# Kernel optimization log

Measured on AMD Instinct MI355X. Metric: run time of the kernel, lower is better.

The kernel has to match this reference:

```python
import jax, jax.numpy as jnp
import numpy as np

FEAT_STRIDE = 16
NUM_ANCHORS = 9
PRE_NMS_TOPN = 6000
POST_NMS_TOPN = 300
NMS_THRESH = 0.7
ANCHOR_SCALES = np.array([8.0, 16.0, 32.0])
ANCHOR_RATIOS = np.array([0.5, 1.0, 2.0])
BBOX_CLIP = float(np.log(1000.0 / 16.0))  # standard delta clip to avoid exp overflow


def _mkanchors(ws, hs, xc, yc):
    return np.stack([xc - 0.5 * (ws - 1), yc - 0.5 * (hs - 1),
                     xc + 0.5 * (ws - 1), yc + 0.5 * (hs - 1)], axis=1)


def _base_anchors(base_size=16):
    w = h = float(base_size)
    xc = yc = 0.5 * (base_size - 1)
    size = w * h
    ws = np.round(np.sqrt(size / ANCHOR_RATIOS))
    hs = np.round(ws * ANCHOR_RATIOS)
    ratio_anchors = _mkanchors(ws, hs, xc, yc)
    out = []
    for a in ratio_anchors:
        aw = a[2] - a[0] + 1.0
        ah = a[3] - a[1] + 1.0
        axc = a[0] + 0.5 * (aw - 1.0)
        ayc = a[1] + 0.5 * (ah - 1.0)
        out.append(_mkanchors(aw * ANCHOR_SCALES, ah * ANCHOR_SCALES, axc, ayc))
    return np.concatenate(out, axis=0)  # [A, 4]


def _all_anchors(H, W):
    base = _base_anchors(FEAT_STRIDE)
    sx = np.arange(W) * FEAT_STRIDE
    sy = np.arange(H) * FEAT_STRIDE
    shift_x, shift_y = np.meshgrid(sx, sy)  # row-major over (h, w)
    shifts = np.stack([shift_x.ravel(), shift_y.ravel(),
                       shift_x.ravel(), shift_y.ravel()], axis=1)
    return (shifts[:, None, :] + base[None, :, :]).reshape(-1, 4).astype(np.float32)


def _conv2d(x, w, b, pad):
    y = jax.lax.conv_general_dilated(x, w, (1, 1), [(pad, pad), (pad, pad)],
                                     dimension_numbers=("NCHW", "OIHW", "NCHW"))
    return y + b[None, :, None, None]


def _decode_clip(anchors, deltas, im_h, im_w):
    aw = anchors[:, 2] - anchors[:, 0] + 1.0
    ah = anchors[:, 3] - anchors[:, 1] + 1.0
    acx = anchors[:, 0] + 0.5 * aw
    acy = anchors[:, 1] + 0.5 * ah
    dx, dy = deltas[:, 0], deltas[:, 1]
    dw = jnp.clip(deltas[:, 2], -BBOX_CLIP, BBOX_CLIP)
    dh = jnp.clip(deltas[:, 3], -BBOX_CLIP, BBOX_CLIP)
    pcx = dx * aw + acx
    pcy = dy * ah + acy
    pw = jnp.exp(dw) * aw
    ph = jnp.exp(dh) * ah
    x1 = jnp.clip(pcx - 0.5 * pw, 0.0, im_w - 1.0)
    y1 = jnp.clip(pcy - 0.5 * ph, 0.0, im_h - 1.0)
    x2 = jnp.clip(pcx + 0.5 * pw, 0.0, im_w - 1.0)
    y2 = jnp.clip(pcy + 0.5 * ph, 0.0, im_h - 1.0)
    return jnp.stack([x1, y1, x2, y2], axis=1)


def _nms_suppressed(boxes, thresh):
    # boxes sorted by score descending; greedy NMS, returns bool suppression mask
    n = boxes.shape[0]
    idx = jnp.arange(n)
    areas = (boxes[:, 2] - boxes[:, 0] + 1.0) * (boxes[:, 3] - boxes[:, 1] + 1.0)
    def body(i, supp):
        b = boxes[i]
        iw = jnp.maximum(0.0, jnp.minimum(b[2], boxes[:, 2]) - jnp.maximum(b[0], boxes[:, 0]) + 1.0)
        ih = jnp.maximum(0.0, jnp.minimum(b[3], boxes[:, 3]) - jnp.maximum(b[1], boxes[:, 1]) + 1.0)
        inter = iw * ih
        iou = inter / (areas[i] + areas - inter)
        kill = (~supp[i]) & (iou > thresh) & (idx > i)
        return supp | kill
    return jax.lax.fori_loop(0, n, body, jnp.zeros((n,), jnp.bool_))


def reference(feature, im_info, w_rpn_conv, b_rpn_conv, w_score, b_score, w_bbox, b_bbox):
    N, C, H, W = feature.shape
    A = NUM_ANCHORS
    rpn_feat = _conv2d(feature, w_rpn_conv, b_rpn_conv, 1)             # [N,512,H,W]
    cls_logits = _conv2d(rpn_feat, w_score, b_score, 0)                # [N,2A,H,W]
    # _reshape_layer(x,2) + softmax(dim=1) + _reshape_layer(x,2A): channels [0:A]=bg, [A:2A]=fg
    fg_prob = jax.nn.softmax(cls_logits.reshape(N, 2, A, H, W), axis=1)[:, 1]  # [N,A,H,W]
    scores = fg_prob.transpose(0, 2, 3, 1).reshape(-1)                 # (h,w,a) order, matches anchors
    deltas = _conv2d(rpn_feat, w_bbox, b_bbox, 0).transpose(0, 2, 3, 1).reshape(-1, 4)
    anchors = jnp.asarray(_all_anchors(H, W))                          # [H*W*A, 4]
    im_h = im_info[0].astype(jnp.float32)
    im_w = im_info[1].astype(jnp.float32)
    proposals = _decode_clip(anchors, deltas, im_h, im_w)
    top_scores, order = jax.lax.top_k(scores, PRE_NMS_TOPN)            # sorted desc
    boxes = proposals[order]
    supp = _nms_suppressed(jax.lax.stop_gradient(boxes), NMS_THRESH)
    masked = jnp.where(supp, -1.0, jax.lax.stop_gradient(top_scores))
    _, keep = jax.lax.top_k(masked, POST_NMS_TOPN)                     # first POST_NMS survivors
    rois_boxes = boxes[keep]                                           # [300, 4]
    roi_scores = top_scores[keep][:, None]                             # [300, 1]
    rois = jnp.concatenate([jnp.zeros((POST_NMS_TOPN, 1), rois_boxes.dtype), rois_boxes], axis=1)
    return rois, roi_scores, feature


def setup_inputs() -> dict:
    key = jax.random.key(0)
    ks = jax.random.split(key, 4)
    C, H, W, A = 512, 128, 128, NUM_ANCHORS
    feature = jax.random.normal(ks[0], (1, C, H, W), jnp.float32)
    w_rpn_conv = jax.random.normal(ks[1], (512, C, 3, 3), jnp.float32) * 0.01
    b_rpn_conv = jnp.zeros((512,), jnp.float32)
    w_score = jax.random.normal(ks[2], (2 * A, 512, 1, 1), jnp.float32) * 0.01
    b_score = jnp.zeros((2 * A,), jnp.float32)
    w_bbox = jax.random.normal(ks[3], (4 * A, 512, 1, 1), jnp.float32) * 0.001
    b_bbox = jnp.zeros((4 * A,), jnp.float32)
    im_info = jnp.array([H * FEAT_STRIDE, W * FEAT_STRIDE, 1], jnp.int32)
    return {"feature": feature, "im_info": im_info,
            "w_rpn_conv": w_rpn_conv, "b_rpn_conv": b_rpn_conv,
            "w_score": w_score, "b_score": b_score,
            "w_bbox": w_bbox, "b_bbox": b_bbox}
```

## Files before the change

kernel.cpp:

```cpp
#include <hip/hip_runtime.h>
#include <hip/hip_bf16.h>


#define HH 128
#define WW 128
#define HW 16384
#define CC 512
#define NANCH 9
#define NTOT 147456
#define PRE_TOPN 6000
#define POST_TOPN 300
#define NMS_WORDS 94
#define CAND_CAP 16384

typedef unsigned int u32;
typedef unsigned long long u64;

__constant__ float c_anch[9][4] = {
  { -84.f,  -40.f,  99.f,  55.f},
  {-176.f,  -88.f, 191.f, 103.f},
  {-360.f, -184.f, 375.f, 199.f},
  { -56.f,  -56.f,  71.f,  71.f},
  {-120.f, -120.f, 135.f, 135.f},
  {-248.f, -248.f, 263.f, 263.f},
  { -36.f,  -80.f,  51.f,  95.f},
  { -80.f, -168.f,  95.f, 183.f},
  {-168.f, -344.f, 183.f, 351.f}
};

__global__ __launch_bounds__(256, 4)
void conv3x3(const float* __restrict__ feat, const float* __restrict__ wconv,
             const float* __restrict__ bias, float* __restrict__ out)
{
  __shared__ float sA[8][3][136];
  __shared__ float sW[72][64];
  const int tid  = threadIdx.x;
  const int oc0  = (blockIdx.x & 7) << 6;
  const int r    = blockIdx.x >> 3;
  const int ocg  = tid >> 4;
  const int p    = tid & 15;

  if (tid < 48) {
    int ic = tid / 6, rm = tid % 6;
    sA[ic][rm >> 1][(rm & 1) ? 132 : 3] = 0.f;
  }

  double acc[4][8];
  #pragma unroll
  for (int o = 0; o < 4; ++o) {
    double bv = (double)bias[oc0 + ocg * 4 + o];
    #pragma unroll
    for (int j = 0; j < 8; ++j) acc[o][j] = bv;
  }

  for (int ic0 = 0; ic0 < CC; ic0 += 8) {
    __syncthreads();
    #pragma unroll
    for (int k = 0; k < 3; ++k) {
      int s   = tid + 256 * k;
      int icr = s >> 5;
      int ic  = icr / 3, rr = icr % 3;
      int c4  = (s & 31) << 2;
      int grow = r - 1 + rr;
      float4 v = make_float4(0.f, 0.f, 0.f, 0.f);
      if (grow >= 0 && grow < HH)
        v = *reinterpret_cast<const float4*>(&feat[(ic0 + ic) * HW + grow * WW + c4]);
      *reinterpret_cast<float4*>(&sA[ic][rr][4 + c4]) = v;
    }
    {
      int oc = tid & 63, part = tid >> 6;
      const float* wp = &wconv[(size_t)((oc0 + oc) * CC + ic0) * 9 + part * 18];
      #pragma unroll
      for (int k = 0; k < 18; ++k) sW[part * 18 + k][oc] = wp[k];
    }
    __syncthreads();

    for (int ic = 0; ic < 8; ++ic) {
      #pragma unroll
      for (int ky = 0; ky < 3; ++ky) {
        double w[3][4];
        #pragma unroll
        for (int kx = 0; kx < 3; ++kx)
          #pragma unroll
          for (int o = 0; o < 4; ++o)
            w[kx][o] = (double)sW[ic * 9 + ky * 3 + kx][ocg * 4 + o];
        const float* arow = &sA[ic][ky][4];
        #pragma unroll
        for (int j = 0; j < 8; ++j) {
          int c = p + 16 * j;
          double a0 = (double)arow[c - 1];
          double a1 = (double)arow[c];
          double a2 = (double)arow[c + 1];
          #pragma unroll
          for (int o = 0; o < 4; ++o) {
            acc[o][j] = fma(a0, w[0][o], acc[o][j]);
            acc[o][j] = fma(a1, w[1][o], acc[o][j]);
            acc[o][j] = fma(a2, w[2][o], acc[o][j]);
          }
        }
      }
    }
  }

  #pragma unroll
  for (int o = 0; o < 4; ++o) {
    float* op = &out[(size_t)(oc0 + ocg * 4 + o) * HW + r * WW];
    #pragma unroll
    for (int j = 0; j < 8; ++j)
      op[p + 16 * j] = (float)acc[o][j];
  }
}

__global__ __launch_bounds__(256, 2)
void conv1x1_decode(const float* __restrict__ rfeat, const float* __restrict__ wsc,
                    const float* __restrict__ bsc, const float* __restrict__ wbb,
                    const float* __restrict__ bbb, const int* __restrict__ im_info,
                    float* __restrict__ scores, double4* __restrict__ props,
                    u32* __restrict__ hist)
{
  __shared__ float  sA[32][64];
  __shared__ float  sW[32][56];
  __shared__ double sOut[64][56];
  const int tid  = threadIdx.x;
  const int px0  = blockIdx.x * 64;
  const int q    = tid >> 6;
  const int px_l = tid & 63;
  const int o0   = q * 14;

  double acc[14];
  #pragma unroll
  for (int o = 0; o < 14; ++o) {
    int oo = o0 + o;
    float b = 0.f;
    if (oo < 18) b = bsc[oo];
    else if (oo < 54) b = bbb[oo - 18];
    acc[o] = (double)b;
  }

  for (int ic0 = 0; ic0 < CC; ic0 += 32) {
    __syncthreads();
    #pragma unroll
    for (int k = 0; k < 2; ++k) {
      int s  = tid + 256 * k;
      int ic = s >> 4;
      int c4 = (s & 15) << 2;
      *reinterpret_cast<float4*>(&sA[ic][c4]) =
        *reinterpret_cast<const float4*>(&rfeat[(ic0 + ic) * HW + px0 + c4]);
    }
    for (int idx = tid; idx < 32 * 56; idx += 256) {
      int ic = idx / 56, o = idx % 56;
      float v = 0.f;
      if (o < 18) v = wsc[o * CC + ic0 + ic];
      else if (o < 54) v = wbb[(o - 18) * CC + ic0 + ic];
      sW[ic][o] = v;
    }
    __syncthreads();
    for (int ic = 0; ic < 32; ++ic) {
      double a = (double)sA[ic][px_l];
      #pragma unroll
      for (int o = 0; o < 14; ++o)
        acc[o] = fma(a, (double)sW[ic][o0 + o], acc[o]);
    }
  }
  #pragma unroll
  for (int o = 0; o < 14; ++o) sOut[px_l][o0 + o] = acc[o];
  __syncthreads();

  const double im_h = (double)im_info[0];
  const double im_w = (double)im_info[1];
  const double BCLIP = 4.1351665567423557;
  for (int t = tid; t < 64 * NANCH; t += 256) {
    int pl = t / 9, a = t % 9;
    int gp = px0 + pl;
    double l0 = sOut[pl][a], l1 = sOut[pl][9 + a];
    double sc = 1.0 / (1.0 + exp(l0 - l1));
    float scf = (float)sc;
    int gi = gp * 9 + a;
    scores[gi] = scf;
    atomicAdd(&hist[__float_as_uint(scf) >> 16], 1u);

    double dx = sOut[pl][18 + 4 * a + 0];
    double dy = sOut[pl][18 + 4 * a + 1];
    double dw = sOut[pl][18 + 4 * a + 2];
    double dh = sOut[pl][18 + 4 * a + 3];
    int wq = gp & 127, hq = gp >> 7;
    double ax1 = (double)c_anch[a][0] + 16.0 * wq;
    double ay1 = (double)c_anch[a][1] + 16.0 * hq;
    double ax2 = (double)c_anch[a][2] + 16.0 * wq;
    double ay2 = (double)c_anch[a][3] + 16.0 * hq;
    double aw = ax2 - ax1 + 1.0, ah = ay2 - ay1 + 1.0;
    double acx = ax1 + 0.5 * aw,  acy = ay1 + 0.5 * ah;
    dw = fmin(fmax(dw, -BCLIP), BCLIP);
    dh = fmin(fmax(dh, -BCLIP), BCLIP);
    double pcx = dx * aw + acx, pcy = dy * ah + acy;
    double pw = exp(dw) * aw,   ph = exp(dh) * ah;
    double x1 = fmin(fmax(pcx - 0.5 * pw, 0.0), im_w - 1.0);
    double y1 = fmin(fmax(pcy - 0.5 * ph, 0.0), im_h - 1.0);
    double x2 = fmin(fmax(pcx + 0.5 * pw, 0.0), im_w - 1.0);
    double y2 = fmin(fmax(pcy + 0.5 * ph, 0.0), im_h - 1.0);
    props[gi] = make_double4(x1, y1, x2, y2);
  }
}

__global__ __launch_bounds__(1024)
void scan_hist(const u32* __restrict__ hist, u32* __restrict__ scal)
{
  __shared__ u32 suf[1024];
  const int t = threadIdx.x;
  u32 s = 0;
  for (int k = 0; k < 64; ++k) s += hist[t * 64 + k];
  suf[t] = s;
  __syncthreads();
  for (int off = 1; off < 1024; off <<= 1) {
    u32 v = (t + off < 1024) ? suf[t + off] : 0u;
    __syncthreads();
    suf[t] += v;
    __syncthreads();
  }
  u32 here = suf[t];
  u32 next = (t < 1023) ? suf[t + 1] : 0u;
  if (here >= PRE_TOPN && (t == 1023 || next < PRE_TOPN)) {
    u32 cum = next;
    int T = t * 64;
    for (int b = 63; b >= 0; --b) {
      cum += hist[t * 64 + b];
      if (cum >= PRE_TOPN) { T = t * 64 + b; break; }
    }
    scal[1] = (u32)T;
  }
}

__global__ void compact_cand(const float* __restrict__ scores,
                             u32* __restrict__ scal, u64* __restrict__ cand)
{
  int t = blockIdx.x * 256 + threadIdx.x;
  if (t >= NTOT) return;
  u32 bits = __float_as_uint(scores[t]);
  if ((bits >> 16) >= scal[1]) {
    u32 pos = atomicAdd(&scal[0], 1u);
    if (pos < CAND_CAP)
      cand[pos] = ((u64)bits << 32) | (u64)(0xFFFFFFFFu - (u32)t);
  }
}

__global__ __launch_bounds__(1024)
void sort_topk(const u64* __restrict__ cand, const u32* __restrict__ scal,
               const double4* __restrict__ props, float* __restrict__ tscore,
               double4* __restrict__ boxes)
{
  __shared__ u64 sk[CAND_CAP];
  u32 n = scal[0]; if (n > CAND_CAP) n = CAND_CAP;
  const int SZ = (n <= 8192) ? 8192 : CAND_CAP;
  for (int t = threadIdx.x; t < SZ; t += 1024)
    sk[t] = (t < (int)n) ? cand[t] : 0ull;
  __syncthreads();
  for (int k = 2; k <= SZ; k <<= 1)
    for (int j = k >> 1; j > 0; j >>= 1) {
      for (int t = threadIdx.x; t < SZ; t += 1024) {
        int p = t ^ j;
        if (p > t) {
          u64 va = sk[t], vb = sk[p];
          bool sw = ((t & k) == 0) ? (va < vb) : (va > vb);
          if (sw) { sk[t] = vb; sk[p] = va; }
        }
      }
      __syncthreads();
    }
  for (int t = threadIdx.x; t < PRE_TOPN; t += 1024) {
    u64 key = sk[t];
    u32 idx = 0xFFFFFFFFu - (u32)key;
    tscore[t] = __uint_as_float((u32)(key >> 32));
    boxes[t]  = props[idx];
  }
}

__global__ __launch_bounds__(64)
void nms_mask(const double4* __restrict__ boxes, u64* __restrict__ mask)
{
  const int bi = blockIdx.y, bj = blockIdx.x;
  const int t = threadIdx.x;
  const int i = bi * 64 + t;
  if (bj < bi) { if (i < PRE_TOPN) mask[(u32)i * NMS_WORDS + bj] = 0ull; return; }
  __shared__ double4 cb[64];
  __shared__ double  ca[64];
  const int j0 = bj * 64;
  if (j0 + t < PRE_TOPN) {
    double4 b = boxes[j0 + t];
    cb[t] = b;
    ca[t] = (b.z - b.x + 1.0) * (b.w - b.y + 1.0);
  }
  __syncthreads();
  if (i >= PRE_TOPN) return;
  double4 bb = boxes[i];
  double ai = (bb.z - bb.x + 1.0) * (bb.w - bb.y + 1.0);
  const int jmax = min(64, PRE_TOPN - j0);
  u64 word = 0ull;
  for (int jj = 0; jj < jmax; ++jj) {
    int j = j0 + jj;
    if (j <= i) continue;
    double4 cj = cb[jj];
    double iw = fmin(bb.z, cj.z) - fmax(bb.x, cj.x) + 1.0;
    double ih = fmin(bb.w, cj.w) - fmax(bb.y, cj.y) + 1.0;
    iw = fmax(iw, 0.0); ih = fmax(ih, 0.0);
    double inter = iw * ih;
    double iou = inter / (ai + ca[jj] - inter);
    if (iou > 0.7) word |= (1ull << jj);
  }
  mask[(u32)i * NMS_WORDS + bj] = word;
}

__global__ __launch_bounds__(256)
void nms_finalize(const u64* __restrict__ mask, const double4* __restrict__ boxes,
                  const float* __restrict__ tscore, float* __restrict__ out)
{
  __shared__ u64 rem[NMS_WORDS];
  __shared__ u64 alv[NMS_WORDS];
  __shared__ int rows[68];
  __shared__ int nrows;
  __shared__ int pre[NMS_WORDS + 1];
  __shared__ int keep[POST_TOPN];
  const int tid = threadIdx.x;
  if (tid < NMS_WORDS) rem[tid] = 0ull;
  __syncthreads();

  for (int c = 0; c < NMS_WORDS; ++c) {
    if (tid < 64) {
      int row = c * 64 + tid;
      u64 m = (row < PRE_TOPN) ? mask[(u32)row * NMS_WORDS + c] : 0ull;
      u64 cur = rem[c];
      for (int b = 0; b < 64; ++b) {
        u64 mb = (u64)__shfl((long long)m, b, 64);
        if (!((cur >> b) & 1ull)) cur |= mb;
      }
      if (tid == 0) {
        rem[c] = cur;
        u64 valid = (c == NMS_WORDS - 1) ? ((1ull << 48) - 1ull) : ~0ull;
        alv[c] = (~cur) & valid;
      }
    }
    if (tid == 255) nrows = 0;
    __syncthreads();
    if (tid < 64 && ((alv[c] >> tid) & 1ull))
      rows[atomicAdd(&nrows, 1)] = c * 64 + tid;
    __syncthreads();
    const int nr = nrows;
    if (tid < 4 && nr > 0) rows[nr + tid] = rows[0];
    __syncthreads();
    if (nr > 0) {
      int w = c + 1 + (tid >> 1);
      if (w < NMS_WORDS) {
        const int sl = tid & 1;
        const int G = (nr + 3) >> 2;
        u64 acc = 0ull;
        for (int g = sl; g < G; g += 2) {
          int b = g << 2;
          int r0 = rows[b], r1 = rows[b + 1], r2 = rows[b + 2], r3 = rows[b + 3];
          acc |= mask[(u32)r0 * NMS_WORDS + w] | mask[(u32)r1 * NMS_WORDS + w]
               | mask[(u32)r2 * NMS_WORDS + w] | mask[(u32)r3 * NMS_WORDS + w];
        }
        if (acc) atomicOr((unsigned long long*)&rem[w], (unsigned long long)acc);
      }
    }
    __syncthreads();
  }

  if (tid == 0) {
    int s = 0;
    for (int c = 0; c < NMS_WORDS; ++c) { pre[c] = s; s += __popcll(alv[c]); }
    pre[NMS_WORDS] = s;
  }
  __syncthreads();
  const int total = pre[NMS_WORDS];
  if (tid < NMS_WORDS) {
    int p = pre[tid];
    u64 bits = alv[tid];
    while (bits && p < POST_TOPN) {
      int b = __ffsll(bits) - 1;
      bits &= bits - 1;
      keep[p] = tid * 64 + b;
      ++p;
    }
  }
  __syncthreads();
  if (total < POST_TOPN) {
    if (tid == 0) {
      int p = total;
      for (int c = 0; c < NMS_WORDS && p < POST_TOPN; ++c) {
        u64 valid = (c == NMS_WORDS - 1) ? ((1ull << 48) - 1ull) : ~0ull;
        u64 bits = rem[c] & valid;
        while (bits && p < POST_TOPN) {
          int b = __ffsll(bits) - 1;
          bits &= bits - 1;
          keep[p++] = c * 64 + b;
        }
      }
    }
    __syncthreads();
  }

  for (int t = tid; t < POST_TOPN; t += 256) {
    int r = keep[t];
    double4 b = boxes[r];
    out[t * 5 + 0] = 0.f;
    out[t * 5 + 1] = (float)b.x;
    out[t * 5 + 2] = (float)b.y;
    out[t * 5 + 3] = (float)b.z;
    out[t * 5 + 4] = (float)b.w;
    out[POST_TOPN * 5 + t] = tscore[r];
  }
}

extern "C" void kernel_launch(void* const* d_in, const int* in_sizes, int n_in,
                              void* d_out, int out_size, void* d_ws, size_t ws_size,
                              hipStream_t stream)
{
  const float* feature = (const float*)d_in[0];
  const int*   im_info = (const int*)d_in[1];
  const float* w_conv  = (const float*)d_in[2];
  const float* b_conv  = (const float*)d_in[3];
  const float* w_sc    = (const float*)d_in[4];
  const float* b_sc    = (const float*)d_in[5];
  const float* w_bb    = (const float*)d_in[6];
  const float* b_bb    = (const float*)d_in[7];
  float* out = (float*)d_out;

  char* ws = (char*)d_ws;
  float*   rfeat  = (float*)(ws);
  float*   scores = (float*)(ws + 33554432);
  double4* props  = (double4*)(ws + 34144256);
  u64*     mask   = (u64*)(ws + 34144256);
  u32*     hist   = (u32*)(ws + 38862848);
  u32*     scal   = (u32*)(ws + 39124992);
  u64*     cand   = (u64*)(ws + 39125248);
  float*   tscore = (float*)(ws + 39256320);
  double4* boxes  = (double4*)(ws + 39280384);

  hipMemsetAsync(hist, 0, 65536 * sizeof(u32), stream);
  hipMemsetAsync(scal, 0, 256, stream);

  conv3x3<<<1024, 256, 0, stream>>>(feature, w_conv, b_conv, rfeat);
  conv1x1_decode<<<256, 256, 0, stream>>>(rfeat, w_sc, b_sc, w_bb, b_bb, im_info,
                                          scores, props, hist);
  scan_hist<<<1, 1024, 0, stream>>>(hist, scal);
  compact_cand<<<(NTOT + 255) / 256, 256, 0, stream>>>(scores, scal, cand);
  sort_topk<<<1, 1024, 0, stream>>>(cand, scal, props, tscore, boxes);
  nms_mask<<<dim3(NMS_WORDS, NMS_WORDS), 64, 0, stream>>>(boxes, mask);
  nms_finalize<<<1, 256, 0, stream>>>(mask, boxes, tscore, out);

  hipMemcpyAsync(out + POST_TOPN * 6, feature, (size_t)CC * HW * sizeof(float),
                 hipMemcpyDeviceToDevice, stream);
}
```

Baseline: 2.996 ms.

## Restructure 3x3 conv tiling with double-precision shared tiles and contiguous pixel quads

The FP64 3x3 convolution is retiled so each thread computes 8 output channels by 4 contiguous pixels instead of 4 channels by 8 strided pixels. Inputs and weights are converted to double once when staged into shared memory, with a padded 5-stride layout to limit bank conflicts. The aim is to remove repeated float-to-double conversions in the inner loop and to reuse each loaded activation across more FMAs, with float4 output stores. In exchange it uses a smaller input-channel chunk per barrier, more shared memory, and lower occupancy (launch bounds 4 to 3).

```diff
diff --git a/kernel.cpp b/kernel.cpp
--- a/kernel.cpp
+++ b/kernel.cpp
@@ -28,86 +28,109 @@
   {-168.f, -344.f, 183.f, 351.f}
 };
 
-__global__ __launch_bounds__(256, 4)
+__global__ __launch_bounds__(256, 3)
 void conv3x3(const float* __restrict__ feat, const float* __restrict__ wconv,
              const float* __restrict__ bias, float* __restrict__ out)
 {
-  __shared__ float sA[8][3][136];
-  __shared__ float sW[72][64];
-  const int tid  = threadIdx.x;
-  const int oc0  = (blockIdx.x & 7) << 6;
-  const int r    = blockIdx.x >> 3;
-  const int ocg  = tid >> 4;
-  const int p    = tid & 15;
-
-  if (tid < 48) {
+  __shared__ double sA[4][3][162];
+  __shared__ double sW[36][64];
+  const int tid = threadIdx.x;
+  const int oc0 = (blockIdx.x & 7) << 6;
+  const int r   = blockIdx.x >> 3;
+  const int ocg = tid >> 5;
+  const int p   = tid & 31;
+
+  if (tid < 24) {
     int ic = tid / 6, rm = tid % 6;
-    sA[ic][rm >> 1][(rm & 1) ? 132 : 3] = 0.f;
-  }
-
-  double acc[4][8];
+    sA[ic][rm >> 1][(rm & 1) ? 161 : 0] = 0.0;
+  }
+
+  double acc[8][4];
   #pragma unroll
-  for (int o = 0; o < 4; ++o) {
-    double bv = (double)bias[oc0 + ocg * 4 + o];
+  for (int o = 0; o < 8; ++o) {
+    double bv = (double)bias[oc0 + ocg * 8 + o];
     #pragma unroll
-    for (int j = 0; j < 8; ++j) acc[o][j] = bv;
-  }
-
-  for (int ic0 = 0; ic0 < CC; ic0 += 8) {
+    for (int j = 0; j < 4; ++j) acc[o][j] = bv;
+  }
+
+  for (int ic0 = 0; ic0 < CC; ic0 += 4) {
     __syncthreads();
     #pragma unroll
-    for (int k = 0; k < 3; ++k) {
-      int s   = tid + 256 * k;
-      int icr = s >> 5;
-      int ic  = icr / 3, rr = icr % 3;
-      int c4  = (s & 31) << 2;
-      int grow = r - 1 + rr;
-      float4 v = make_float4(0.f, 0.f, 0.f, 0.f);
-      if (grow >= 0 && grow < HH)
-        v = *reinterpret_cast<const float4*>(&feat[(ic0 + ic) * HW + grow * WW + c4]);
-      *reinterpret_cast<float4*>(&sA[ic][rr][4 + c4]) = v;
+    for (int k = 0; k < 2; ++k) {
+      int s = tid + 256 * k;
+      if (s < 384) {
+        int icr = s >> 5;
+        int ic = icr / 3, rr = icr % 3;
+        int lam = s & 31;
+        int grow = r - 1 + rr;
+        float4 v = make_float4(0.f, 0.f, 0.f, 0.f);
+        if (grow >= 0 && grow < HH)
+          v = *reinterpret_cast<const float4*>(
+                &feat[(ic0 + ic) * HW + grow * WW + lam * 4]);
+        double* dst = &sA[ic][rr][5 * lam];
+        dst[1] = (double)v.x;
+        dst[2] = (double)v.y;
+        dst[3] = (double)v.z;
+        dst[5] = (double)v.w;
+      }
     }
     {
-      int oc = tid & 63, part = tid >> 6;
-      const float* wp = &wconv[(size_t)((oc0 + oc) * CC + ic0) * 9 + part * 18];
+      int part = tid >> 6, oc = tid & 63;
+      const float* wp = &wconv[(size_t)((oc0 + oc) * CC + ic0 + part) * 9];
       #pragma unroll
-      for (int k = 0; k < 18; ++k) sW[part * 18 + k][oc] = wp[k];
-    }
-    __syncthreads();
-
-    for (int ic = 0; ic < 8; ++ic) {
+      for (int t = 0; t < 9; ++t)
+        sW[part * 9 + t][oc] = (double)wp[t];
+    }
+    __syncthreads();
+
+    #pragma unroll
+    for (int ic = 0; ic < 4; ++ic) {
       #pragma unroll
       for (int ky = 0; ky < 3; ++ky) {
-        double w[3][4];
+        const double* arow = &sA[ic][ky][5 * p];
+        double a0 = arow[0];
+        double a1 = arow[1];
+        double a2 = arow[2];
+        double a3 = arow[3];
+        double a4 = arow[5];
+        double a5 = arow[6];
         #pragma unroll
-        for (int kx = 0; kx < 3; ++kx)
-          #pragma unroll
-          for (int o = 0; o < 4; ++o)
-            w[kx][o] = (double)sW[ic * 9 + ky * 3 + kx][ocg * 4 + o];
-        const float* arow = &sA[ic][ky][4];
-        #pragma unroll
-        for (int j = 0; j < 8; ++j) {
-          int c = p + 16 * j;
-          double a0 = (double)arow[c - 1];
-          double a1 = (double)arow[c];
-          double a2 = (double)arow[c + 1];
-          #pragma unroll
-          for (int o = 0; o < 4; ++o) {
-            acc[o][j] = fma(a0, w[0][o], acc[o][j]);
-            acc[o][j] = fma(a1, w[1][o], acc[o][j]);
-            acc[o][j] = fma(a2, w[2][o], acc[o][j]);
-          }
+        for (int kx = 0; kx < 3; ++kx) {
+          const double* wrow = &sW[ic * 9 + ky * 3 + kx][ocg * 8];
+          double w0 = wrow[0], w1 = wrow[1], w2 = wrow[2], w3 = wrow[3];
+          double w4 = wrow[4], w5 = wrow[5], w6 = wrow[6], w7 = wrow[7];
+          double b0, b1, b2, b3;
+          if (kx == 0)      { b0 = a0; b1 = a1; b2 = a2; b3 = a3; }
+          else if (kx == 1) { b0 = a1; b1 = a2; b2 = a3; b3 = a4; }
+          else              { b0 = a2; b1 = a3; b2 = a4; b3 = a5; }
+          acc[0][0] = fma(b0, w0, acc[0][0]); acc[0][1] = fma(b1, w0, acc[0][1]);
+          acc[0][2] = fma(b2, w0, acc[0][2]); acc[0][3] = fma(b3, w0, acc[0][3]);
+          acc[1][0] = fma(b0, w1, acc[1][0]); acc[1][1] = fma(b1, w1, acc[1][1]);
+          acc[1][2] = fma(b2, w1, acc[1][2]); acc[1][3] = fma(b3, w1, acc[1][3]);
+          acc[2][0] = fma(b0, w2, acc[2][0]); acc[2][1] = fma(b1, w2, acc[2][1]);
+          acc[2][2] = fma(b2, w2, acc[2][2]); acc[2][3] = fma(b3, w2, acc[2][3]);
+          acc[3][0] = fma(b0, w3, acc[3][0]); acc[3][1] = fma(b1, w3, acc[3][1]);
+          acc[3][2] = fma(b2, w3, acc[3][2]); acc[3][3] = fma(b3, w3, acc[3][3]);
+          acc[4][0] = fma(b0, w4, acc[4][0]); acc[4][1] = fma(b1, w4, acc[4][1]);
+          acc[4][2] = fma(b2, w4, acc[4][2]); acc[4][3] = fma(b3, w4, acc[4][3]);
+          acc[5][0] = fma(b0, w5, acc[5][0]); acc[5][1] = fma(b1, w5, acc[5][1]);
+          acc[5][2] = fma(b2, w5, acc[5][2]); acc[5][3] = fma(b3, w5, acc[5][3]);
+          acc[6][0] = fma(b0, w6, acc[6][0]); acc[6][1] = fma(b1, w6, acc[6][1]);
+          acc[6][2] = fma(b2, w6, acc[6][2]); acc[6][3] = fma(b3, w6, acc[6][3]);
+          acc[7][0] = fma(b0, w7, acc[7][0]); acc[7][1] = fma(b1, w7, acc[7][1]);
+          acc[7][2] = fma(b2, w7, acc[7][2]); acc[7][3] = fma(b3, w7, acc[7][3]);
         }
       }
     }
   }
 
   #pragma unroll
-  for (int o = 0; o < 4; ++o) {
-    float* op = &out[(size_t)(oc0 + ocg * 4 + o) * HW + r * WW];
-    #pragma unroll
-    for (int j = 0; j < 8; ++j)
-      op[p + 16 * j] = (float)acc[o][j];
+  for (int o = 0; o < 8; ++o) {
+    float4 v;
+    v.x = (float)acc[o][0]; v.y = (float)acc[o][1];
+    v.z = (float)acc[o][2]; v.w = (float)acc[o][3];
+    *reinterpret_cast<float4*>(
+      &out[(size_t)(oc0 + ocg * 8 + o) * HW + r * WW + 4 * p]) = v;
   }
 }
 
```

Result: slower. 3.699 ms (+23.5%).

## Pre-convert conv weights to reordered fp64 and restructure 3x3 conv kernel

Applied to the files above, without the earlier changes.

Adds a weight pre-pass that converts the 3x3 conv weights to double and reorders them per group of 8 output channels, so the conv can read them directly from global memory without LDS staging. The new conv kernel uses 512 threads, each wave handling 8 output channels and each lane two adjacent pixels. Inputs are stored as doubles in padded shared rows to reduce bank conflicts. The old kernel stays as a fallback when the workspace is too small, and the new path adds an extra kernel launch plus a larger workspace footprint that overlaps the scores region.

```diff
diff --git a/kernel.cpp b/kernel.cpp
--- a/kernel.cpp
+++ b/kernel.cpp
@@ -28,9 +28,103 @@
   {-168.f, -344.f, 183.f, 351.f}
 };
 
+__global__ __launch_bounds__(256)
+void wcvt(const float* __restrict__ wconv, double* __restrict__ wd)
+{
+  int idx = blockIdx.x * 256 + threadIdx.x;
+  int t  = idx % 9;
+  int ic = (idx / 9) & 511;
+  int oc = idx / 4608;
+  int g  = oc >> 3, o8 = oc & 7;
+  wd[(size_t)g * 36864 + ic * 72 + t * 8 + o8] = (double)wconv[idx];
+}
+
+__global__ __launch_bounds__(512)
+void conv3x3(const float* __restrict__ feat, const double* __restrict__ wd,
+             const float* __restrict__ bias, float* __restrict__ out)
+{
+  __shared__ double sA[4][3][162];
+  const int tid = threadIdx.x;
+  const int oc0 = (blockIdx.x & 7) << 6;
+  const int r   = blockIdx.x >> 3;
+  const int wv  = __builtin_amdgcn_readfirstlane(tid >> 6);
+  const int l   = tid & 63;
+
+  const int c0 = 2 * l;
+  const int x0 = c0 + (c0 >> 2);
+  const int x1 = (c0 + 1) + ((c0 + 1) >> 2);
+  const int x2 = (c0 + 2) + ((c0 + 2) >> 2);
+  const int x3 = (c0 + 3) + ((c0 + 3) >> 2);
+
+  if (tid < 24) {
+    int ic = tid / 6, rm = tid % 6;
+    sA[ic][rm >> 1][(rm & 1) ? 161 : 0] = 0.0;
+  }
+
+  double acc[8][2];
+  #pragma unroll
+  for (int o = 0; o < 8; ++o) {
+    double bv = (double)bias[oc0 + wv * 8 + o];
+    acc[o][0] = bv; acc[o][1] = bv;
+  }
+
+  const double* wg = wd + (size_t)((oc0 >> 3) + wv) * 36864;
+
+  for (int ic0 = 0; ic0 < CC; ic0 += 4) {
+    __syncthreads();
+    if (tid < 384) {
+      int icr = tid >> 5;
+      int ic = icr / 3, rr = icr % 3;
+      int lam = tid & 31;
+      int grow = r - 1 + rr;
+      float4 v = make_float4(0.f, 0.f, 0.f, 0.f);
+      if (grow >= 0 && grow < HH)
+        v = *reinterpret_cast<const float4*>(
+              &feat[(ic0 + ic) * HW + grow * WW + lam * 4]);
+      double* dst = &sA[ic][rr][5 * lam];
+      dst[1] = (double)v.x;
+      dst[2] = (double)v.y;
+      dst[3] = (double)v.z;
+      dst[5] = (double)v.w;
+    }
+    __syncthreads();
+
+    const double* wc = wg + ic0 * 72;
+    #pragma unroll
+    for (int ic = 0; ic < 4; ++ic) {
+      #pragma unroll
+      for (int ky = 0; ky < 3; ++ky) {
+        const double* arow = sA[ic][ky];
+        double a0 = arow[x0], a1 = arow[x1], a2 = arow[x2], a3 = arow[x3];
+        const double* wp = wc + ic * 72 + ky * 24;
+        #pragma unroll
+        for (int kx = 0; kx < 3; ++kx) {
+          double b0 = (kx == 0) ? a0 : ((kx == 1) ? a1 : a2);
+          double b1 = (kx == 0) ? a1 : ((kx == 1) ? a2 : a3);
+          #pragma unroll
+          for (int o = 0; o < 8; ++o) {
+            double w = wp[kx * 8 + o];
+            acc[o][0] = fma(b0, w, acc[o][0]);
+            acc[o][1] = fma(b1, w, acc[o][1]);
+          }
+        }
+      }
+    }
+  }
+
+  #pragma unroll
+  for (int o = 0; o < 8; ++o) {
+    float2 v;
+    v.x = (float)acc[o][0];
+    v.y = (float)acc[o][1];
+    *reinterpret_cast<float2*>(
+      &out[(size_t)(oc0 + wv * 8 + o) * HW + r * WW + 2 * l]) = v;
+  }
+}
+
 __global__ __launch_bounds__(256, 4)
-void conv3x3(const float* __restrict__ feat, const float* __restrict__ wconv,
-             const float* __restrict__ bias, float* __restrict__ out)
+void conv3x3_fb(const float* __restrict__ feat, const float* __restrict__ wconv,
+                const float* __restrict__ bias, float* __restrict__ out)
 {
   __shared__ float sA[8][3][136];
   __shared__ float sW[72][64];
@@ -426,6 +520,7 @@
 
   char* ws = (char*)d_ws;
   float*   rfeat  = (float*)(ws);
+  double*  wd     = (double*)(ws + 33554432);
   float*   scores = (float*)(ws + 33554432);
   double4* props  = (double4*)(ws + 34144256);
   u64*     mask   = (u64*)(ws + 34144256);
@@ -435,10 +530,17 @@
   float*   tscore = (float*)(ws + 39256320);
   double4* boxes  = (double4*)(ws + 39280384);
 
+  const bool big = (ws_size >= 52428800ull);
+  if (big) {
+    wcvt<<<9216, 256, 0, stream>>>(w_conv, wd);
+    conv3x3<<<1024, 512, 0, stream>>>(feature, wd, b_conv, rfeat);
+  } else {
+    conv3x3_fb<<<1024, 256, 0, stream>>>(feature, w_conv, b_conv, rfeat);
+  }
+
   hipMemsetAsync(hist, 0, 65536 * sizeof(u32), stream);
   hipMemsetAsync(scal, 0, 256, stream);
 
-  conv3x3<<<1024, 256, 0, stream>>>(feature, w_conv, b_conv, rfeat);
   conv1x1_decode<<<256, 256, 0, stream>>>(rfeat, w_sc, b_sc, w_bb, b_bb, im_info,
                                           scores, props, hist);
   scan_hist<<<1, 1024, 0, stream>>>(hist, scal);
```

Measured after the change: 2.815 ms. -6.0%, faster.
